# Kernel optimization log

Hardware: AMD Instinct MI355X
Metric: run time of the kernel (lower is better)

The kernel has to match this reference:

```python
import jax, jax.numpy as jnp
import numpy as np

B, L, H = 2, 4096, 1024


def _rope_tables(seq_len, dim, base=10000.0):
    # standard RoPE cos/sin tables, rotate-half convention, shape [L, dim]
    inv_freq = 1.0 / (base ** (np.arange(0, dim, 2, dtype=np.float32) / dim))
    t = np.arange(seq_len, dtype=np.float32)
    freqs = np.outer(t, inv_freq)                      # [L, dim/2]
    emb = np.concatenate([freqs, freqs], axis=-1)      # [L, dim]
    return jnp.asarray(np.cos(emb)), jnp.asarray(np.sin(emb))


def setup_inputs() -> dict:
    key = jax.random.key(0)
    k1, k2 = jax.random.split(key)
    hidden_states = jax.random.normal(k1, (B, L, H), dtype=jnp.float32)
    # queries weight: normal with std = initializer_range / sqrt(2*num_layers*hidden)
    std = 0.02 / np.sqrt(2.0 * 24 * H)
    W_q = jax.random.normal(k2, (H, H), dtype=jnp.float32) * std
    cos, sin = _rope_tables(L, H)
    return {"hidden_states": hidden_states, "W_q": W_q, "cos": cos, "sin": sin}


def _rotate_half(x):
    x1, x2 = jnp.split(x, 2, axis=-1)
    return jnp.concatenate([-x2, x1], axis=-1)


def reference(hidden_states, W_q, cos, sin):
    # dropout with p=0.0 (eval) -> identity
    h = hidden_states * cos[None, :, :] + _rotate_half(hidden_states) * sin[None, :, :]  # RoPE, [B,L,H]
    q = jnp.einsum('blh,oh->blo', h, W_q)          # F.linear(h, W_q), [B,L,H]
    pre_attn = jnp.einsum('blh,bmh->blm', q, h)    # Q @ K^T (no softmax), [B,L,L]
    attention = jnp.einsum('blm,bmh->blh', pre_attn, h)  # scores @ V, [B,L,H]
    return attention
```

## Files before the change

### kernel.cpp

```cpp
#include <hip/hip_runtime.h>
#include <hip/hip_bf16.h>
#include <stdint.h>

#define BB 2
#define LL 4096
#define HH 1024
#define GBK 32

typedef __bf16 bf16;
typedef __bf16 bf16x4 __attribute__((ext_vector_type(4)));
typedef __bf16 bf16x8 __attribute__((ext_vector_type(8)));
typedef float  f32x4  __attribute__((ext_vector_type(4)));

__device__ __forceinline__ void async_cp16(const bf16* g, const bf16* l)
{
    typedef const uint32_t __attribute__((address_space(1)))* gp_t;
    typedef uint32_t __attribute__((address_space(3)))* lp_t;
    __builtin_amdgcn_global_load_lds((gp_t)(uintptr_t)g, (lp_t)(uintptr_t)l, 16, 0, 0);
}

__global__ __launch_bounds__(128) void rope_kernel(
    const float* __restrict__ x, const float* __restrict__ cs,
    const float* __restrict__ sn, bf16* __restrict__ h)
{
    const int l = blockIdx.x;
    const int b = blockIdx.y;
    const int i = threadIdx.x * 4;
    const long xb = ((long)b * LL + l) * HH;
    const long cb = (long)l * HH;

    const float4 x1 = *(const float4*)(x + xb + i);
    const float4 x2 = *(const float4*)(x + xb + i + HH / 2);
    const float4 c1 = *(const float4*)(cs + cb + i);
    const float4 c2 = *(const float4*)(cs + cb + i + HH / 2);
    const float4 s1 = *(const float4*)(sn + cb + i);
    const float4 s2 = *(const float4*)(sn + cb + i + HH / 2);

    bf16x4 o1, o2;
    o1[0] = (bf16)(x1.x * c1.x - x2.x * s1.x);
    o1[1] = (bf16)(x1.y * c1.y - x2.y * s1.y);
    o1[2] = (bf16)(x1.z * c1.z - x2.z * s1.z);
    o1[3] = (bf16)(x1.w * c1.w - x2.w * s1.w);
    o2[0] = (bf16)(x2.x * c2.x + x1.x * s2.x);
    o2[1] = (bf16)(x2.y * c2.y + x1.y * s2.y);
    o2[2] = (bf16)(x2.z * c2.z + x1.z * s2.z);
    o2[3] = (bf16)(x2.w * c2.w + x1.w * s2.w);

    *(bf16x4*)(h + xb + i)          = o1;
    *(bf16x4*)(h + xb + i + HH / 2) = o2;
}

__global__ __launch_bounds__(256) void transpose_bf16_64(
    const bf16* __restrict__ in, bf16* __restrict__ out, const int R, const int C)
{
    __shared__ uint32_t lds[64][36];
    const long zoff = (long)blockIdx.z * R * C;
    const int r0 = blockIdx.x * 64;
    const int c0 = blockIdx.y * 64;
    const int t  = threadIdx.x;

    const int c8 = t & 7;
    const int rr = t >> 3;
    const bf16* p0 = in + zoff + (long)(r0 + 2 * rr) * C + c0 + c8 * 8;
    const uint4 ra = *(const uint4*)p0;
    const uint4 rb = *(const uint4*)(p0 + C);
    const uint32_t av[4] = {ra.x, ra.y, ra.z, ra.w};
    const uint32_t bv[4] = {rb.x, rb.y, rb.z, rb.w};
#pragma unroll
    for (int j = 0; j < 4; ++j) {
        const uint32_t alo = av[j] & 0xffffu, ahi = av[j] >> 16;
        const uint32_t blo = bv[j] & 0xffffu, bhi = bv[j] >> 16;
        lds[c8 * 8 + 2 * j    ][rr] = alo | (blo << 16);
        lds[c8 * 8 + 2 * j + 1][rr] = ahi | (bhi << 16);
    }
    __syncthreads();

    const int c = t >> 2;
    const int q = t & 3;
    const uint4 w0 = *(const uint4*)&lds[c][q * 8];
    const uint4 w1 = *(const uint4*)&lds[c][q * 8 + 4];
    bf16* po = out + zoff + (long)(c0 + c) * R + r0 + q * 16;
    *(uint4*)(po)     = w0;
    *(uint4*)(po + 8) = w1;
}

__global__ __launch_bounds__(256) void cast_wq(
    const float* __restrict__ Wq, bf16* __restrict__ Wb)
{
    const long idx = ((long)blockIdx.x * 256 + threadIdx.x) * 4;
    const float4 v = *(const float4*)(Wq + idx);
    bf16x4 o;
    o[0] = (bf16)v.x; o[1] = (bf16)v.y; o[2] = (bf16)v.z; o[3] = (bf16)v.w;
    *(bf16x4*)(Wb + idx) = o;
}

#define GEMM_SHARED()                                                          \
    __shared__ __align__(16) bf16 As[2][128][32];                              \
    __shared__ __align__(16) bf16 Bs[2][128][32];

#define GEMM_PREFETCH(KOFF, BUF)                                               \
    do {                                                                       \
        async_cp16(Ag + (KOFF),           &As[BUF][0][0] + woff0);             \
        async_cp16(Ag + (KOFF) + 64L * K, &As[BUF][0][0] + woff1);             \
        async_cp16(Bg + (KOFF),           &Bs[BUF][0][0] + woff0);             \
        async_cp16(Bg + (KOFF) + 64L * K, &Bs[BUF][0][0] + woff1);             \
    } while (0)

#define GEMM_BODY(M0, N0, KBASE, KEND, DST, DT, LDN)                           \
    {                                                                          \
        const int tid  = threadIdx.x;                                          \
        const int lane = tid & 63;                                             \
        const int wave = tid >> 6;                                             \
        const int wm = (wave & 1) * 64;                                        \
        const int wn = (wave >> 1) * 64;                                       \
        const int fr = lane & 15;                                              \
        const int fq = lane >> 4;                                              \
        const int srow = tid >> 2;                                             \
        const int scol = (tid & 3) * 8;                                        \
        const int woff0 = wave * 512;                  \
        const int woff1 = 2048 + wave * 512;           \
        const bf16* Ag = Ab + (long)((M0) + srow) * K + scol;                  \
        const bf16* Bg = Bb + (long)((N0) + srow) * K + scol;                  \
        const f32x4 vzero = {0.f, 0.f, 0.f, 0.f};                              \
        f32x4 acc[4][4];                                                       \
        _Pragma("unroll") for (int i = 0; i < 4; ++i)                          \
            _Pragma("unroll") for (int j = 0; j < 4; ++j) acc[i][j] = vzero;   \
        GEMM_PREFETCH(KBASE, 0);                                               \
        int buf = 0;                                                           \
        for (int k0 = (KBASE); k0 < (KEND); k0 += GBK, buf ^= 1) {             \
            __syncthreads();                    \
            if (k0 + GBK < (KEND)) GEMM_PREFETCH(k0 + GBK, buf ^ 1);           \
            bf16x8 af[4], bfv[4];                                              \
            _Pragma("unroll") for (int i = 0; i < 4; ++i)                      \
                af[i]  = *(const bf16x8*)&As[buf][wm + i * 16 + fr][fq * 8];   \
            _Pragma("unroll") for (int j = 0; j < 4; ++j)                      \
                bfv[j] = *(const bf16x8*)&Bs[buf][wn + j * 16 + fr][fq * 8];   \
            _Pragma("unroll") for (int i = 0; i < 4; ++i)                      \
                _Pragma("unroll") for (int j = 0; j < 4; ++j)                  \
                    acc[i][j] = __builtin_amdgcn_mfma_f32_16x16x32_bf16(       \
                        af[i], bfv[j], acc[i][j], 0, 0, 0);                    \
        }                                                                      \
             \
        _Pragma("unroll") for (int i = 0; i < 4; ++i) {                        \
            _Pragma("unroll") for (int r = 0; r < 4; ++r) {                    \
                const int row = (M0) + wm + i * 16 + fq * 4 + r;               \
                _Pragma("unroll") for (int j = 0; j < 4; ++j) {                \
                    const int col = (N0) + wn + j * 16 + fr;                   \
                    (DST)[(long)row * (LDN) + col] = (DT)acc[i][j][r];         \
                }                                                              \
            }                                                                  \
        }                                                                      \
    }

template <typename OUT_T>
__global__ __launch_bounds__(256) void gemm_bt(
    const bf16* __restrict__ A, const bf16* __restrict__ B, OUT_T* __restrict__ C,
    const int M, const int N, const int K,
    const long sA, const long sB, const long sC)
{
    GEMM_SHARED();
    const bf16* Ab = A + blockIdx.z * sA;
    const bf16* Bb = B + blockIdx.z * sB;
    OUT_T*      Cb = C + blockIdx.z * sC;
    const int m0 = blockIdx.x * 128;
    const int n0 = blockIdx.y * 128;
    GEMM_BODY(m0, n0, 0, K, Cb, OUT_T, N);
}

__global__ __launch_bounds__(256) void gemm_Gq(
    const bf16* __restrict__ hT, const bf16* __restrict__ Wb,
    const bf16* __restrict__ h, float* __restrict__ P, bf16* __restrict__ q)
{
    GEMM_SHARED();
    const int id = blockIdx.x;
    if (id < 512) {
        const int plane = id >> 6;
        const int zb = plane >> 2;
        const int zs = plane & 3;
        const int t  = id & 63;
        const int m0 = (t & 7) * 128;
        const int n0 = (t >> 3) * 128;
        const bf16* Ab = hT + (long)zb * HH * LL;
        const bf16* Bb = Ab;
        float* Cb = P + (long)plane * HH * HH;
        const int K = LL;
        const int kbase = zs * (LL / 4);
        GEMM_BODY(m0, n0, kbase, kbase + LL / 4, Cb, float, HH);
    } else {
        const int t  = id - 512;
        const int m0 = (t & 63) * 128;
        const int n0 = (t >> 6) * 128;
        const bf16* Ab = h;
        const bf16* Bb = Wb;
        const int K = HH;
        GEMM_BODY(m0, n0, 0, HH, q, bf16, HH);
    }
}

__global__ __launch_bounds__(256) void reduce_splits(
    const float* __restrict__ P, bf16* __restrict__ out, const int npb, const int S)
{
    const int b = blockIdx.y;
    const long r = ((long)blockIdx.x * 256 + threadIdx.x) * 4;
    const float* base = P + (long)b * S * npb + r;
    float4 a = *(const float4*)(base);
    for (int s = 1; s < S; ++s) {
        const float4 v = *(const float4*)(base + (long)s * npb);
        a.x += v.x; a.y += v.y; a.z += v.z; a.w += v.w;
    }
    bf16x4 o;
    o[0] = (bf16)a.x; o[1] = (bf16)a.y; o[2] = (bf16)a.z; o[3] = (bf16)a.w;
    *(bf16x4*)(out + (long)b * npb + r) = o;
}

extern "C" void kernel_launch(void* const* d_in, const int* in_sizes, int n_in,
                              void* d_out, int out_size, void* d_ws, size_t ws_size,
                              hipStream_t stream)
{
    const float* x  = (const float*)d_in[0];
    const float* Wq = (const float*)d_in[1];
    const float* cs = (const float*)d_in[2];
    const float* sn = (const float*)d_in[3];
    float* out = (float*)d_out;
    char* ws = (char*)d_ws;

    bf16*  h  = (bf16*)(ws);
    bf16*  hT = (bf16*)(ws + 16u * 1024 * 1024);
    bf16*  Wb = (bf16*)(ws + 32u * 1024 * 1024);
    bf16*  G  = (bf16*)(ws + 34u * 1024 * 1024);
    float* P  = (float*)(ws + 38u * 1024 * 1024);

    const bool big_ws = ws_size >= (size_t)90 * 1024 * 1024;
    bf16* q = big_ws ? (bf16*)(ws + 70u * 1024 * 1024)
                     : (bf16*)(ws + 38u * 1024 * 1024);

    rope_kernel<<<dim3(LL, BB), 128, 0, stream>>>(x, cs, sn, h);

    transpose_bf16_64<<<dim3(LL / 64, HH / 64, BB), 256, 0, stream>>>(h, hT, LL, HH);

    cast_wq<<<dim3(HH * HH / 1024), 256, 0, stream>>>(Wq, Wb);

    if (big_ws) {
        gemm_Gq<<<dim3(1024), 256, 0, stream>>>(hT, Wb, h, P, q);
        reduce_splits<<<dim3(HH * HH / 1024, BB), 256, 0, stream>>>(P, G, HH * HH, 4);
    } else {
        gemm_bt<bf16><<<dim3(HH / 128, HH / 128, BB), 256, 0, stream>>>(
            hT, hT, G, HH, HH, LL, (long)HH * LL, (long)HH * LL, (long)HH * HH);
        gemm_bt<bf16><<<dim3(LL / 128, HH / 128, BB), 256, 0, stream>>>(
            h, Wb, q, LL, HH, HH, (long)LL * HH, 0L, (long)LL * HH);
    }

    gemm_bt<float><<<dim3(LL / 128, HH / 128, BB), 256, 0, stream>>>(
        q, G, out, LL, HH, HH, (long)LL * HH, (long)HH * HH, (long)LL * HH);
}
```

Before: 195.6 us.

## Replace GEMM kernels with 256x256-tile 8-wave pipelined MFMA engine

Adds a new GEMM engine with 256x256 block tiles, 512 threads (8 waves), and a 64-wide K stage. Shared memory is XOR-swizzled and split into halves so that async global-to-LDS loads for later K tiles interleave with MFMA quadrants under explicit barriers and waitcnts. It also raises wave priority around the MFMA blocks. The engine is used for both the fused G/q GEMM and the final q·G GEMM on the big-workspace path. The intent is more data reuse per tile and overlap of loads with compute. The cost is fewer blocks (128–256, which may underfill 256 CUs), higher register pressure, and fragile hand scheduling.

```diff
diff --git a/kernel.cpp b/kernel.cpp
--- a/kernel.cpp
+++ b/kernel.cpp
@@ -95,15 +95,15 @@
 }
 
 #define GEMM_SHARED()                                                          \
-    __shared__ __align__(16) bf16 As[2][128][32];                              \
-    __shared__ __align__(16) bf16 Bs[2][128][32];
+    __shared__ __align__(16) bf16 As_[2][128][32];                             \
+    __shared__ __align__(16) bf16 Bs_[2][128][32];
 
 #define GEMM_PREFETCH(KOFF, BUF)                                               \
     do {                                                                       \
-        async_cp16(Ag + (KOFF),           &As[BUF][0][0] + woff0);             \
-        async_cp16(Ag + (KOFF) + 64L * K, &As[BUF][0][0] + woff1);             \
-        async_cp16(Bg + (KOFF),           &Bs[BUF][0][0] + woff0);             \
-        async_cp16(Bg + (KOFF) + 64L * K, &Bs[BUF][0][0] + woff1);             \
+        async_cp16(Ag + (KOFF),           &As_[BUF][0][0] + woff0);            \
+        async_cp16(Ag + (KOFF) + 64L * K, &As_[BUF][0][0] + woff1);            \
+        async_cp16(Bg + (KOFF),           &Bs_[BUF][0][0] + woff0);            \
+        async_cp16(Bg + (KOFF) + 64L * K, &Bs_[BUF][0][0] + woff1);            \
     } while (0)
 
 #define GEMM_BODY(M0, N0, KBASE, KEND, DST, DT, LDN)                           \
@@ -117,8 +117,8 @@
         const int fq = lane >> 4;                                              \
         const int srow = tid >> 2;                                             \
         const int scol = (tid & 3) * 8;                                        \
-        const int woff0 = wave * 512;                  \
-        const int woff1 = 2048 + wave * 512;           \
+        const int woff0 = wave * 512;                                          \
+        const int woff1 = 2048 + wave * 512;                                   \
         const bf16* Ag = Ab + (long)((M0) + srow) * K + scol;                  \
         const bf16* Bg = Bb + (long)((N0) + srow) * K + scol;                  \
         const f32x4 vzero = {0.f, 0.f, 0.f, 0.f};                              \
@@ -128,19 +128,18 @@
         GEMM_PREFETCH(KBASE, 0);                                               \
         int buf = 0;                                                           \
         for (int k0 = (KBASE); k0 < (KEND); k0 += GBK, buf ^= 1) {             \
-            __syncthreads();                    \
+            __syncthreads();                                                   \
             if (k0 + GBK < (KEND)) GEMM_PREFETCH(k0 + GBK, buf ^ 1);           \
             bf16x8 af[4], bfv[4];                                              \
             _Pragma("unroll") for (int i = 0; i < 4; ++i)                      \
-                af[i]  = *(const bf16x8*)&As[buf][wm + i * 16 + fr][fq * 8];   \
+                af[i]  = *(const bf16x8*)&As_[buf][wm + i * 16 + fr][fq * 8];  \
             _Pragma("unroll") for (int j = 0; j < 4; ++j)                      \
-                bfv[j] = *(const bf16x8*)&Bs[buf][wn + j * 16 + fr][fq * 8];   \
+                bfv[j] = *(const bf16x8*)&Bs_[buf][wn + j * 16 + fr][fq * 8];  \
             _Pragma("unroll") for (int i = 0; i < 4; ++i)                      \
                 _Pragma("unroll") for (int j = 0; j < 4; ++j)                  \
                     acc[i][j] = __builtin_amdgcn_mfma_f32_16x16x32_bf16(       \
                         af[i], bfv[j], acc[i][j], 0, 0, 0);                    \
         }                                                                      \
-             \
         _Pragma("unroll") for (int i = 0; i < 4; ++i) {                        \
             _Pragma("unroll") for (int r = 0; r < 4; ++r) {                    \
                 const int row = (M0) + wm + i * 16 + fq * 4 + r;               \
@@ -167,34 +166,177 @@
     GEMM_BODY(m0, n0, 0, K, Cb, OUT_T, N);
 }
 
-__global__ __launch_bounds__(256) void gemm_Gq(
+#define E_STAGE_A(KT, PART, BUF)                                               \
+  do {                                                                         \
+    const int kk0_ = kbase + (KT) * 64;                                        \
+    _Pragma("unroll") for (int qq_ = 0; qq_ < 2; ++qq_) {                      \
+      const int ch_  = qq_ * 512 + tid;                                        \
+      const int sl_  = ch_ >> 3;                                               \
+      const int cc_  = (ch_ & 7) ^ (sl_ & 7);                                  \
+      const int row_ = (sl_ & 63) + (PART) * 64 + ((sl_ >> 6) << 7);           \
+      async_cp16(Ab + (long)(m0 + row_) * K + kk0_ + cc_ * 8,                  \
+                 &As[BUF][PART][0][0] + (qq_ * 512 + (tid & 448)) * 8);        \
+    }                                                                          \
+  } while (0)
+
+#define E_STAGE_B(KT, PART, BUF)                                               \
+  do {                                                                         \
+    const int kk0_ = kbase + (KT) * 64;                                        \
+    _Pragma("unroll") for (int qq_ = 0; qq_ < 2; ++qq_) {                      \
+      const int ch_  = qq_ * 512 + tid;                                        \
+      const int sl_  = ch_ >> 3;                                               \
+      const int cc_  = (ch_ & 7) ^ (sl_ & 7);                                  \
+      const int row_ = (sl_ & 31) + (PART) * 32 + ((sl_ >> 5) << 6);           \
+      async_cp16(Bb + (long)(n0 + row_) * K + kk0_ + cc_ * 8,                  \
+                 &Bs[BUF][PART][0][0] + (qq_ * 512 + (tid & 448)) * 8);        \
+    }                                                                          \
+  } while (0)
+
+#define E_LOAD_A(BUF, IG)                                                      \
+  do {                                                                         \
+    const bf16* Ap_ = &As[BUF][IG][0][0] + (wr * 64 + fr) * 64;                \
+    _Pragma("unroll") for (int ii_ = 0; ii_ < 4; ++ii_)                        \
+      _Pragma("unroll") for (int kk_ = 0; kk_ < 2; ++kk_)                      \
+        af[ii_][kk_] = *(const bf16x8*)(Ap_ + ii_ * 1024 +                     \
+                        (((kk_ * 4 + fq) ^ fr7) * 8));                         \
+  } while (0)
+
+#define E_LOAD_B(BUF, JP)                                                      \
+  do {                                                                         \
+    const bf16* Bp_ = &Bs[BUF][JP][0][0] + (wc * 32 + fr) * 64;                \
+    _Pragma("unroll") for (int jj_ = 0; jj_ < 2; ++jj_)                        \
+      _Pragma("unroll") for (int kk_ = 0; kk_ < 2; ++kk_)                      \
+        bfv[jj_][kk_] = *(const bf16x8*)(Bp_ + jj_ * 1024 +                    \
+                        (((kk_ * 4 + fq) ^ fr7) * 8));                         \
+  } while (0)
+
+#define E_MMA(IG, JG)                                                          \
+  do {                                                                         \
+    __builtin_amdgcn_s_setprio(1);                                             \
+    _Pragma("unroll") for (int ii_ = 0; ii_ < 4; ++ii_)                        \
+      _Pragma("unroll") for (int jj_ = 0; jj_ < 2; ++jj_)                      \
+        _Pragma("unroll") for (int kk_ = 0; kk_ < 2; ++kk_)                    \
+          acc[(IG) * 4 + ii_][(JG) * 2 + jj_] =                                \
+              __builtin_amdgcn_mfma_f32_16x16x32_bf16(                         \
+                  af[ii_][kk_], bfv[jj_][kk_],                                 \
+                  acc[(IG) * 4 + ii_][(JG) * 2 + jj_], 0, 0, 0);               \
+    __builtin_amdgcn_s_setprio(0);                                             \
+  } while (0)
+
+#define E_BAR()   __builtin_amdgcn_s_barrier()
+#define E_LGKM0() do { asm volatile("s_waitcnt lgkmcnt(0)" ::: "memory");      \
+                       __builtin_amdgcn_sched_barrier(0); } while (0)
+#define E_VM(N)   asm volatile("s_waitcnt vmcnt(" #N ")" ::: "memory")
+
+#define ENGINE_PREAMBLE()                                                      \
+  __shared__ __align__(16) bf16 As[2][2][128][64];                             \
+  __shared__ __align__(16) bf16 Bs[2][2][128][64];                             \
+  const int tid  = threadIdx.x;                                                \
+  const int lane = tid & 63;                                                   \
+  const int wv   = tid >> 6;                                                   \
+  const int wr   = wv >> 2;                                                    \
+  const int wc   = wv & 3;                                                     \
+  const int fr   = lane & 15;                                                  \
+  const int fq   = lane >> 4;                                                  \
+  const int fr7  = fr & 7;                                                     \
+  bf16x8 af[4][2], bfv[2][2];                                                  \
+  f32x4 acc[8][4];                                                             \
+  _Pragma("unroll") for (int i_ = 0; i_ < 8; ++i_)                             \
+    _Pragma("unroll") for (int j_ = 0; j_ < 4; ++j_)                           \
+      acc[i_][j_] = (f32x4){0.f, 0.f, 0.f, 0.f};
+
+#define ENGINE_LOOP(NT)                                                        \
+    \
+  E_STAGE_A(0, 0, 0); E_STAGE_B(0, 1, 0); E_STAGE_A(0, 1, 0);                  \
+  E_STAGE_B(0, 0, 0);                                                          \
+  E_STAGE_A(1, 0, 1); E_STAGE_B(1, 1, 1); E_STAGE_A(1, 1, 1);                  \
+  E_VM(6); E_BAR();                                                            \
+  int t_ = 0;                                                                  \
+  _Pragma("unroll 1") for (; t_ + 3 < (NT); t_ += 2) {                         \
+     E_LOAD_A(0, 0); E_LOAD_B(0, 0); E_STAGE_B(t_ + 1, 0, 1);          \
+             E_BAR(); E_LGKM0(); E_MMA(0, 0); E_BAR();                         \
+     E_LOAD_B(0, 1); E_STAGE_A(t_ + 2, 0, 0);                          \
+             E_BAR(); E_LGKM0(); E_MMA(0, 1); E_BAR();                         \
+     E_LOAD_A(0, 1); E_STAGE_B(t_ + 2, 1, 0);                          \
+             E_BAR(); E_LGKM0(); E_MMA(1, 1); E_BAR();                         \
+     E_LOAD_B(0, 0); E_STAGE_A(t_ + 2, 1, 0);                          \
+             E_BAR(); E_LGKM0(); E_MMA(1, 0); E_VM(6); E_BAR();                \
+     E_LOAD_A(1, 0); E_LOAD_B(1, 0); E_STAGE_B(t_ + 2, 0, 0);          \
+             E_BAR(); E_LGKM0(); E_MMA(0, 0); E_BAR();                         \
+     E_LOAD_B(1, 1); E_STAGE_A(t_ + 3, 0, 1);                          \
+             E_BAR(); E_LGKM0(); E_MMA(0, 1); E_BAR();                         \
+     E_LOAD_A(1, 1); E_STAGE_B(t_ + 3, 1, 1);                          \
+             E_BAR(); E_LGKM0(); E_MMA(1, 1); E_BAR();                         \
+     E_LOAD_B(1, 0); E_STAGE_A(t_ + 3, 1, 1);                          \
+             E_BAR(); E_LGKM0(); E_MMA(1, 0); E_VM(6); E_BAR();                \
+  }                                                                            \
+                  \
+  E_LOAD_A(0, 0); E_LOAD_B(0, 0); E_STAGE_B(t_ + 1, 0, 1);                     \
+  E_BAR(); E_LGKM0(); E_MMA(0, 0); E_BAR();                                    \
+  E_LOAD_B(0, 1); E_BAR(); E_LGKM0(); E_MMA(0, 1); E_BAR();                    \
+  E_LOAD_A(0, 1); E_BAR(); E_LGKM0(); E_MMA(1, 1); E_BAR();                    \
+  E_LOAD_B(0, 0); E_BAR(); E_LGKM0(); E_MMA(1, 0); E_VM(0); E_BAR();           \
+  E_LOAD_A(1, 0); E_LOAD_B(1, 0); E_BAR(); E_LGKM0(); E_MMA(0, 0); E_BAR();    \
+  E_LOAD_B(1, 1); E_BAR(); E_LGKM0(); E_MMA(0, 1); E_BAR();                    \
+  E_LOAD_A(1, 1); E_BAR(); E_LGKM0(); E_MMA(1, 1); E_BAR();                    \
+  E_LOAD_B(1, 0); E_BAR(); E_LGKM0(); E_MMA(1, 0);
+
+#define ENGINE_STORE(DST, DT, LDN)                                             \
+  _Pragma("unroll") for (int gi_ = 0; gi_ < 8; ++gi_) {                        \
+    _Pragma("unroll") for (int r_ = 0; r_ < 4; ++r_) {                         \
+      const int row_ = m0 + wr * 128 + gi_ * 16 + fq * 4 + r_;                 \
+      _Pragma("unroll") for (int gj_ = 0; gj_ < 4; ++gj_) {                    \
+        const int col_ = n0 + wc * 64 + gj_ * 16 + fr;                         \
+        (DST)[(long)row_ * (LDN) + col_] = (DT)acc[gi_][gj_][r_];              \
+      }                                                                        \
+    }                                                                          \
+  }
+
+__global__ __launch_bounds__(512, 2) void gemm8_Gq(
     const bf16* __restrict__ hT, const bf16* __restrict__ Wb,
     const bf16* __restrict__ h, float* __restrict__ P, bf16* __restrict__ q)
 {
-    GEMM_SHARED();
+    ENGINE_PREAMBLE();
     const int id = blockIdx.x;
-    if (id < 512) {
-        const int plane = id >> 6;
-        const int zb = plane >> 2;
-        const int zs = plane & 3;
-        const int t  = id & 63;
-        const int m0 = (t & 7) * 128;
-        const int n0 = (t >> 3) * 128;
-        const bf16* Ab = hT + (long)zb * HH * LL;
-        const bf16* Bb = Ab;
-        float* Cb = P + (long)plane * HH * HH;
-        const int K = LL;
-        const int kbase = zs * (LL / 4);
-        GEMM_BODY(m0, n0, kbase, kbase + LL / 4, Cb, float, HH);
+    const bf16* Ab; const bf16* Bb;
+    int K, kbase, m0, n0;
+    float* Pc = nullptr;
+    if (id < 128) {
+        m0 = (id & 31) * 256;
+        n0 = (id >> 5) * 256;
+        Ab = h; Bb = Wb; K = HH; kbase = 0;
     } else {
-        const int t  = id - 512;
-        const int m0 = (t & 63) * 128;
-        const int n0 = (t >> 6) * 128;
-        const bf16* Ab = h;
-        const bf16* Bb = Wb;
-        const int K = HH;
-        GEMM_BODY(m0, n0, 0, HH, q, bf16, HH);
-    }
+        const int u  = id - 128;
+        const int zb = u >> 6;
+        const int v  = u & 63;
+        const int zs = v >> 4;
+        const int tl = v & 15;
+        m0 = (tl & 3) * 256;
+        n0 = (tl >> 2) * 256;
+        Ab = hT + (long)zb * HH * LL; Bb = Ab;
+        K  = LL; kbase = zs * (LL / 4);
+        Pc = P + (long)(zb * 4 + zs) * HH * HH;
+    }
+    ENGINE_LOOP(16);
+    if (Pc) { ENGINE_STORE(Pc, float, HH); }
+    else    { ENGINE_STORE(q,  bf16,  HH); }
+}
+
+__global__ __launch_bounds__(512, 2) void gemm8_qG(
+    const bf16* __restrict__ q, const bf16* __restrict__ G, float* __restrict__ out)
+{
+    ENGINE_PREAMBLE();
+    const int id = blockIdx.x;
+    const int b  = id >> 6;
+    const int u  = id & 63;
+    const int m0 = (u & 15) * 256;
+    const int n0 = (u >> 4) * 256;
+    const bf16* Ab = q + (long)b * LL * HH;
+    const bf16* Bb = G + (long)b * HH * HH;
+    const int K = HH, kbase = 0;
+    float* outb = out + (long)b * LL * HH;
+    ENGINE_LOOP(16);
+    ENGINE_STORE(outb, float, HH);
 }
 
 __global__ __launch_bounds__(256) void reduce_splits(
@@ -241,15 +383,15 @@
     cast_wq<<<dim3(HH * HH / 1024), 256, 0, stream>>>(Wq, Wb);
 
     if (big_ws) {
-        gemm_Gq<<<dim3(1024), 256, 0, stream>>>(hT, Wb, h, P, q);
+        gemm8_Gq<<<dim3(256), 512, 0, stream>>>(hT, Wb, h, P, q);
         reduce_splits<<<dim3(HH * HH / 1024, BB), 256, 0, stream>>>(P, G, HH * HH, 4);
+        gemm8_qG<<<dim3(128), 512, 0, stream>>>(q, G, out);
     } else {
         gemm_bt<bf16><<<dim3(HH / 128, HH / 128, BB), 256, 0, stream>>>(
             hT, hT, G, HH, HH, LL, (long)HH * LL, (long)HH * LL, (long)HH * HH);
         gemm_bt<bf16><<<dim3(LL / 128, HH / 128, BB), 256, 0, stream>>>(
             h, Wb, q, LL, HH, HH, (long)LL * HH, 0L, (long)LL * HH);
-    }
-
-    gemm_bt<float><<<dim3(LL / 128, HH / 128, BB), 256, 0, stream>>>(
-        q, G, out, LL, HH, HH, (long)LL * HH, (long)HH * HH, (long)LL * HH);
-}
+        gemm_bt<float><<<dim3(LL / 128, HH / 128, BB), 256, 0, stream>>>(
+            q, G, out, LL, HH, HH, (long)LL * HH, (long)HH * HH, (long)LL * HH);
+    }
+}
```

Result: faster. 190.9 us (-2.4%).
